# Optimization experiments

Hardware: AMD Instinct MI355X
Metric: run time of the kernel (lower is better)

The kernel has to match this reference:

```python
import jax, jax.numpy as jnp
import numpy as np

B, S, E = 4, 1024, 1024   # batch, seq_len, emb_dim
H = 8                      # num_head
D = E                      # in_emb_dim defaults to emb_dim
NEG = -9e15                # source uses -9000000000000000.0


def setup_inputs() -> dict:
    key = jax.random.key(0)
    kq, kk, kv, kwq, kwk, kwv, kwl = jax.random.split(key, 7)
    q = jax.random.normal(kq, (B, S, E), dtype=jnp.float32)
    k = jax.random.normal(kk, (B, S, E), dtype=jnp.float32)
    v = jax.random.normal(kv, (B, S, E), dtype=jnp.float32)
    # Per-head Linear(emb_dim -> in_emb_dim, bias=False) weights, torch layout [out, in]
    Wq = jax.random.normal(kwq, (H, D, E), dtype=jnp.float32) * 0.02
    Wk = jax.random.normal(kwk, (H, D, E), dtype=jnp.float32) * 0.02
    Wv = jax.random.normal(kwv, (H, D, E), dtype=jnp.float32) * 0.02
    # last_dense: Linear(in_emb_dim*num_head -> emb_dim, bias=False)
    Wlast = jax.random.normal(kwl, (E, H * D), dtype=jnp.float32) * 0.02
    return {"q": q, "k": k, "v": v, "Wq": Wq, "Wk": Wk, "Wv": Wv, "Wlast": Wlast}


def reference(q, k, v, Wq, Wk, Wv, Wlast):
    # batched per-head projections: y = x @ W[h].T  -> [B,H,S,D]
    in_q = jnp.einsum('bse,hde->bhsd', q, Wq)
    in_k = jnp.einsum('bse,hde->bhsd', k, Wk)
    in_v = jnp.einsum('bse,hde->bhsd', v, Wv)
    # faithful: scaled by sqrt(kv sequence length), not head dim
    scale = 1.0 / jnp.sqrt(jnp.float32(k.shape[-2]))
    logits = jnp.einsum('bhqd,bhkd->bhqk', in_q, in_k) * scale
    # source maps exactly-zero logits to -9e15 before softmax
    logits = jnp.where(logits != 0, logits, jnp.full_like(logits, NEG))
    atten = jax.nn.softmax(logits, axis=-1)          # [B,H,Sq,Sk]
    out_h = jnp.einsum('bhqk,bhkd->bhqd', atten, in_v)
    # concat heads along last dim in head order (matches torch.cat loop)
    b, h, sq, d = out_h.shape
    h_cat = out_h.transpose(0, 2, 1, 3).reshape(b, sq, h * d)
    return jnp.einsum('bsf,ef->bse', h_cat, Wlast)   # last_dense, bias=False
```

## Files before the change

### kernel.cpp

```cpp
#include <hip/hip_runtime.h>
#include <stdint.h>

typedef _Float16 f16;
typedef _Float16 f16x8 __attribute__((ext_vector_type(8)));
typedef _Float16 f16x4 __attribute__((ext_vector_type(4)));
typedef float f32x4 __attribute__((ext_vector_type(4)));

__device__ __forceinline__ void gload_lds16(const void* g, void* l) {
    __builtin_amdgcn_global_load_lds(
        (const __attribute__((address_space(1))) unsigned int*)g,
        (__attribute__((address_space(3))) unsigned int*)l, 16, 0, 0);
}

#define VMWAIT0() asm volatile("s_waitcnt vmcnt(0)" ::: "memory")
#define LGKM0()   asm volatile("s_waitcnt lgkmcnt(0)" ::: "memory")

struct Cvt3 {
    const float* s[3];
    f16* d[3];
};
__global__ __launch_bounds__(256) void cvt_plain3(Cvt3 c) {
    const int seg = blockIdx.y;
    const int i = blockIdx.x * 256 + threadIdx.x;
    const float4* s4 = (const float4*)c.s[seg];
    float4 a = s4[2 * (size_t)i];
    float4 b = s4[2 * (size_t)i + 1];
    f16x8 o;
    o[0] = (f16)a.x; o[1] = (f16)a.y; o[2] = (f16)a.z; o[3] = (f16)a.w;
    o[4] = (f16)b.x; o[5] = (f16)b.y; o[6] = (f16)b.z; o[7] = (f16)b.w;
    *(f16x8*)(c.d[seg] + (size_t)i * 8) = o;
}

__global__ __launch_bounds__(256) void cvt_wl(const float* __restrict__ s,
                                              f16* __restrict__ d) {
    const int i = blockIdx.x * 256 + threadIdx.x;
    const int d8 = i & 127;
    const int e  = (i >> 7) & 1023;
    const int h  = i >> 17;
    const float4* s4 = (const float4*)(s + (size_t)e * 8192 + h * 1024 + d8 * 8);
    float4 a = s4[0], b = s4[1];
    f16x8 o;
    o[0] = (f16)a.x; o[1] = (f16)a.y; o[2] = (f16)a.z; o[3] = (f16)a.w;
    o[4] = (f16)b.x; o[5] = (f16)b.y; o[6] = (f16)b.z; o[7] = (f16)b.w;
    *(f16x8*)(d + (size_t)i * 8) = o;
}

struct T3 { const float* s[3]; f16* d[3]; };
__global__ __launch_bounds__(256) void cvt_transpose3(T3 c) {
    const int bid = blockIdx.x;
    const int dt = bid & 15;
    const int et = (bid >> 4) & 15;
    const int zz = bid >> 8;
    const int m = zz >> 3, h = zz & 7;
    const float* src = c.s[m] + (size_t)h * 1048576;
    f16* dst = c.d[m] + (size_t)h * 1048576;
    __shared__ f16 t[64][72];
    const int r  = threadIdx.x >> 2;
    const int cq = threadIdx.x & 3;
    const int d0 = dt * 64, e0 = et * 64;
#pragma unroll
    for (int i = 0; i < 4; ++i) {
        const int cc = cq * 4 + i * 16;
        float4 vv = *(const float4*)(src + (size_t)(d0 + r) * 1024 + e0 + cc);
        t[cc + 0][r] = (f16)vv.x;
        t[cc + 1][r] = (f16)vv.y;
        t[cc + 2][r] = (f16)vv.z;
        t[cc + 3][r] = (f16)vv.w;
    }
    __syncthreads();
#pragma unroll
    for (int i = 0; i < 4; ++i) {
        const int cc = cq * 4 + i * 16;
        f16x4 w;
        w[0] = t[r][cc + 0];
        w[1] = t[r][cc + 1];
        w[2] = t[r][cc + 2];
        w[3] = t[r][cc + 3];
        *(f16x4*)(dst + (size_t)(e0 + r) * 1024 + d0 + cc) = w;
    }
}

template <typename OutT>
__global__ __launch_bounds__(256, 2) void gemm_bt(
    const f16* __restrict__ A, const f16* __restrict__ B, OutT* __restrict__ C,
    int ldA, int ldB, long long ldC, int K, float alpha,
    long long sAh, long long sAb, long long sBh, long long sBb,
    long long sCh, long long sCb, int NB, int gx, int gy) {
    const int nwg = gridDim.x;
    const int q = nwg >> 3, r = nwg & 7;
    const int xcd = blockIdx.x & 7, lid = blockIdx.x >> 3;
    const int wg = (xcd < r ? xcd * (q + 1) : r * (q + 1) + (xcd - r) * q) + lid;
    const int z = wg / (gx * gy);
    const int rem = wg - z * (gx * gy);
    const int by = rem / gx, bx = rem - by * gx;
    const int h = z / NB, bb = z % NB;
    A += h * sAh + bb * sAb;
    B += h * sBh + bb * sBb;
    C += h * sCh + bb * sCb;

    const int row0 = by * 128;
    const int col0 = bx * 128;

    __shared__ __align__(16) f16 smA[128 * 64];
    __shared__ __align__(16) f16 smB[128 * 64];

    const int tid  = threadIdx.x;
    const int lane = tid & 63;
    const int wid  = tid >> 6;
    const int wr   = (wid >> 1) * 64;
    const int wc   = (wid & 1) * 64;
    const int fr   = lane & 15;
    const int fkb  = (lane >> 4) * 16;

    f32x4 acc[4][4] = {};

    const int nkt = K >> 6;
    for (int kt = 0; kt < nkt; ++kt) {
#pragma unroll
        for (int it = 0; it < 4; ++it) {
            int p = (it * 256 + tid) * 16;
            int n = p ^ (((p >> 7) & 7) << 4);
            int rr  = n >> 7;
            int kel = (n & 127) >> 1;
            size_t ga = (size_t)(row0 + rr) * (size_t)ldA + (size_t)(kt * 64 + kel);
            gload_lds16(A + ga, (char*)smA + p);
            size_t gb = (size_t)(col0 + rr) * (size_t)ldB + (size_t)(kt * 64 + kel);
            gload_lds16(B + gb, (char*)smB + p);
        }
        __syncthreads();

#pragma unroll
        for (int ks = 0; ks < 2; ++ks) {
            f16x8 af[4], bf[4];
#pragma unroll
            for (int i = 0; i < 4; ++i) {
                int rowA = wr + i * 16 + fr;
                int na   = rowA * 128 + ks * 64 + fkb;
                af[i] = *(const f16x8*)((const char*)smA + (na ^ ((rowA & 7) << 4)));
                int rowB = wc + i * 16 + fr;
                int nb   = rowB * 128 + ks * 64 + fkb;
                bf[i] = *(const f16x8*)((const char*)smB + (nb ^ ((rowB & 7) << 4)));
            }
#pragma unroll
            for (int i = 0; i < 4; ++i)
#pragma unroll
                for (int j = 0; j < 4; ++j)
                    acc[i][j] = __builtin_amdgcn_mfma_f32_16x16x32_f16(
                        af[i], bf[j], acc[i][j], 0, 0, 0);
        }
        __syncthreads();
    }

    const int er = (lane >> 4) * 4;
#pragma unroll
    for (int i = 0; i < 4; ++i)
#pragma unroll
        for (int j = 0; j < 4; ++j)
#pragma unroll
            for (int rr = 0; rr < 4; ++rr) {
                size_t idx = (size_t)(row0 + wr + i * 16 + er + rr) * (size_t)ldC +
                             (size_t)(col0 + wc + j * 16 + fr);
                C[idx] = (OutT)(acc[i][j][rr] * alpha);
            }
}

template <typename OutT>
__global__ __launch_bounds__(512, 2) void gemm2ph(
    const f16* __restrict__ A, const f16* __restrict__ B, OutT* __restrict__ C,
    int ldA, int ldB, long long ldC, int K, float alpha,
    long long sAh, long long sAb, long long sBh, long long sBb,
    long long sCh, long long sCb, int NB, int gx, int gy) {
    extern __shared__ char lds[];

    const int nwg = gridDim.x;
    const int q = nwg >> 3, r = nwg & 7;
    const int xcd = blockIdx.x & 7, lid = blockIdx.x >> 3;
    const int wg = (xcd < r ? xcd * (q + 1) : r * (q + 1) + (xcd - r) * q) + lid;
    const int z = wg / (gx * gy);
    const int rem = wg - z * (gx * gy);
    const int by = rem / gx, bx = rem - by * gx;
    const int h = z / NB, bb = z - h * NB;
    A += h * sAh + bb * sAb;
    B += h * sBh + bb * sBb;
    C += h * sCh + bb * sCb;
    const int row0 = by * 256, col0 = bx * 256;

    const int tid  = threadIdx.x;
    const int lane = tid & 63;
    const int wid  = tid >> 6;
    const int wm   = wid >> 2;
    const int wn   = wid & 3;
    const int fr   = lane & 15;
    const int fkb  = (lane >> 4) << 4;
    const int sw0  = fkb ^ ((fr & 7) << 4);
    const int sw1  = sw0 ^ 64;

    const unsigned ldsbase = (unsigned)(uintptr_t)(char*)lds;
    const unsigned aRow = ldsbase + (unsigned)((wm * 128 + fr) * 128);
    const unsigned bRow = ldsbase + 32768u + (unsigned)((wn * 64 + fr) * 128);

    const int srow  = tid >> 3;
    const int scol  = (((tid & 7) ^ ((tid >> 3) & 7)) << 4) >> 1;
    const f16* gA = A + (size_t)(row0 + srow) * ldA + scol;
    const f16* gB = B + (size_t)(col0 + srow) * ldB + scol;
    char* lA = (char*)lds + tid * 16;
    char* lB = lA + 32768;

    const int nkt = K >> 6;

#define STAGE(tt, bufo) do { \
        const size_t _ko = (size_t)(tt) * 64; \
        gload_lds16(gA + _ko,                        lA + (bufo)); \
        gload_lds16(gA + 64  * (size_t)ldA + _ko,    lA + (bufo) + 8192); \
        gload_lds16(gA + 128 * (size_t)ldA + _ko,    lA + (bufo) + 16384); \
        gload_lds16(gA + 192 * (size_t)ldA + _ko,    lA + (bufo) + 24576); \
        gload_lds16(gB + _ko,                        lB + (bufo)); \
        gload_lds16(gB + 64  * (size_t)ldB + _ko,    lB + (bufo) + 8192); \
        gload_lds16(gB + 128 * (size_t)ldB + _ko,    lB + (bufo) + 16384); \
        gload_lds16(gB + 192 * (size_t)ldB + _ko,    lB + (bufo) + 24576); \
    } while (0)

#define DSR2(r0, r1, addr, o0, o1) \
    asm volatile("ds_read_b128 %0, %2 offset:" #o0 "\n\t" \
                 "ds_read_b128 %1, %2 offset:" #o1 \
                 : "=&v"(r0), "=&v"(r1) : "v"(addr))

#define MF(i, j, av, bv) \
    acc[i][j] = __builtin_amdgcn_mfma_f32_16x16x32_f16(av, bv, acc[i][j], 0, 0, 0)

#define HALF(sw) do { \
        f16x8 a0, a1, a2, a3, a4, a5, a6, a7, b0, b1, b2, b3; \
        const unsigned aA = aRow + bo + (sw); \
        const unsigned aB = bRow + bo + (sw); \
        DSR2(a0, a1, aA, 0, 2048); \
        DSR2(a2, a3, aA, 4096, 6144); \
        DSR2(a4, a5, aA, 8192, 10240); \
        DSR2(a6, a7, aA, 12288, 14336); \
        DSR2(b0, b1, aB, 0, 2048); \
        DSR2(b2, b3, aB, 4096, 6144); \
        LGKM0(); \
        __builtin_amdgcn_sched_barrier(0); \
        __builtin_amdgcn_s_setprio(1); \
        MF(0,0,a0,b0); MF(0,1,a0,b1); MF(0,2,a0,b2); MF(0,3,a0,b3); \
        MF(1,0,a1,b0); MF(1,1,a1,b1); MF(1,2,a1,b2); MF(1,3,a1,b3); \
        MF(2,0,a2,b0); MF(2,1,a2,b1); MF(2,2,a2,b2); MF(2,3,a2,b3); \
        MF(3,0,a3,b0); MF(3,1,a3,b1); MF(3,2,a3,b2); MF(3,3,a3,b3); \
        MF(4,0,a4,b0); MF(4,1,a4,b1); MF(4,2,a4,b2); MF(4,3,a4,b3); \
        MF(5,0,a5,b0); MF(5,1,a5,b1); MF(5,2,a5,b2); MF(5,3,a5,b3); \
        MF(6,0,a6,b0); MF(6,1,a6,b1); MF(6,2,a6,b2); MF(6,3,a6,b3); \
        MF(7,0,a7,b0); MF(7,1,a7,b1); MF(7,2,a7,b2); MF(7,3,a7,b3); \
        __builtin_amdgcn_s_setprio(0); \
    } while (0)

    STAGE(0, 0);
    VMWAIT0();
    __builtin_amdgcn_s_barrier();

    f32x4 acc[8][4] = {};
    unsigned cur = 0;

    for (int t = 0; t < nkt; ++t) {
        const unsigned bo = cur << 16;
        if (t + 1 < nkt) STAGE(t + 1, bo ^ 65536u);
        HALF(sw0);
        HALF(sw1);
        VMWAIT0();
        __builtin_amdgcn_s_barrier();
        cur ^= 1;
    }
#undef HALF
#undef MF
#undef DSR2
#undef STAGE

    const int er = (lane >> 4) * 4;
#pragma unroll
    for (int i = 0; i < 8; ++i)
#pragma unroll
        for (int j = 0; j < 4; ++j)
#pragma unroll
            for (int rr = 0; rr < 4; ++rr) {
                size_t idx = (size_t)(row0 + wm * 128 + i * 16 + er + rr) * (size_t)ldC +
                             (size_t)(col0 + wn * 64 + j * 16 + fr);
                C[idx] = (OutT)(acc[i][j][rr] * alpha);
            }
}

__global__ __launch_bounds__(256) void reduce_split2(const float* __restrict__ p,
                                                     float* __restrict__ o, int n4) {
    int i = blockIdx.x * 256 + threadIdx.x;
    if (i >= n4) return;
    const int b  = i >> 18;
    const int jj = i & 262143;
    const float4* p4 = (const float4*)p;
    const size_t base = (size_t)b * 524288 + jj;
    float4 a = p4[base], c = p4[base + 262144];
    float4 s;
    s.x = a.x + c.x;
    s.y = a.y + c.y;
    s.z = a.z + c.z;
    s.w = a.w + c.w;
    ((float4*)o)[i] = s;
}

__global__ __launch_bounds__(256) void softmax_rows(f16* __restrict__ P) {
    const size_t row = blockIdx.x;
    f16* p = P + row * 1024;
    const int tid = threadIdx.x, lane = tid & 63, wid = tid >> 6;

    f16x4 v4 = *(const f16x4*)(p + tid * 4);
    float v[4];
#pragma unroll
    for (int t = 0; t < 4; ++t) {
        v[t] = (float)v4[t];
        if (v[t] == 0.0f) v[t] = -9e15f;
    }
    float m = fmaxf(fmaxf(v[0], v[1]), fmaxf(v[2], v[3]));
#pragma unroll
    for (int o = 32; o > 0; o >>= 1) m = fmaxf(m, __shfl_xor(m, o));
    __shared__ float red[8];
    if (lane == 0) red[wid] = m;
    __syncthreads();
    m = fmaxf(fmaxf(red[0], red[1]), fmaxf(red[2], red[3]));

    float e[4], s = 0.f;
#pragma unroll
    for (int t = 0; t < 4; ++t) { e[t] = __expf(v[t] - m); s += e[t]; }
#pragma unroll
    for (int o = 32; o > 0; o >>= 1) s += __shfl_xor(s, o);
    if (lane == 0) red[4 + wid] = s;
    __syncthreads();
    s = red[4] + red[5] + red[6] + red[7];
    float inv = 1.0f / s;

    f16x4 o4;
#pragma unroll
    for (int t = 0; t < 4; ++t) o4[t] = (f16)(e[t] * inv);
    *(f16x4*)(p + tid * 4) = o4;
}

extern "C" void kernel_launch(void* const* d_in, const int* in_sizes, int n_in,
                              void* d_out, int out_size, void* d_ws, size_t ws_size,
                              hipStream_t stream) {
    const float* q  = (const float*)d_in[0];
    const float* k  = (const float*)d_in[1];
    const float* v  = (const float*)d_in[2];
    const float* Wq = (const float*)d_in[3];
    const float* Wk = (const float*)d_in[4];
    const float* Wv = (const float*)d_in[5];
    const float* Wl = (const float*)d_in[6];
    float* out = (float*)d_out;

    (void)hipFuncSetAttribute((const void*)gemm2ph<f16>,
                              hipFuncAttributeMaxDynamicSharedMemorySize, 131072);

    const size_t MB = 1024ull * 1024ull;
    char* ws = (char*)d_ws;
    f16*  q_h  = (f16*)(ws + 0 * MB);
    f16*  k_h  = (f16*)(ws + 8 * MB);
    f16*  v_h  = (f16*)(ws + 16 * MB);
    f16*  WkT  = (f16*)(ws + 24 * MB);
    f16*  Wl_r = (f16*)(ws + 40 * MB);
    f16*  WqT  = (f16*)(ws + 56 * MB);
    f16*  WvT  = (f16*)(ws + 72 * MB);
    f16*  Mt   = (f16*)(ws + 88 * MB);
    f16*  G    = (f16*)(ws + 104 * MB);
    f16*  Aq   = (f16*)(ws + 24 * MB);
    f16*  P    = (f16*)(ws + 120 * MB);
    f16*  Xt   = (f16*)(ws + 24 * MB);
    float* part = (float*)(ws + 88 * MB);

    Cvt3 c3;
    c3.s[0] = q;  c3.d[0] = q_h;
    c3.s[1] = k;  c3.d[1] = k_h;
    c3.s[2] = v;  c3.d[2] = v_h;
    cvt_plain3<<<dim3(2048, 3), 256, 0, stream>>>(c3);
    cvt_wl<<<4096, 256, 0, stream>>>(Wl, Wl_r);

    T3 t3;
    t3.s[0] = Wq; t3.d[0] = WqT;
    t3.s[1] = Wk; t3.d[1] = WkT;
    t3.s[2] = Wv; t3.d[2] = WvT;
    cvt_transpose3<<<6144, 256, 0, stream>>>(t3);

    const long long M1 = 1048576ll;
    const long long M8 = 8388608ll;
    const float SCALE = 0.03125f;
    const size_t SMEM = 131072;

    gemm2ph<f16><<<256, 512, SMEM, stream>>>(
        WkT, WqT, Mt, 1024, 1024, 1024, 1024, 1.0f,
        M1, 0, M1, 0, M1, 0, 1, 4, 4);
    gemm2ph<f16><<<512, 512, SMEM, stream>>>(
        q_h, Mt, Aq, 1024, 1024, 1024, 1024, 1.0f,
        0, M1, M1, 0, 4 * M1, M1, 4, 4, 4);
    gemm2ph<f16><<<512, 512, SMEM, stream>>>(
        Aq, k_h, P, 1024, 1024, 8192, 1024, SCALE,
        4 * M1, M1, 0, M1, 1024, M8, 4, 4, 4);
    gemm2ph<f16><<<512, 512, SMEM, stream>>>(
        G, v_h, Xt, 1024, 1024, 8192, 1024, 1.0f,
        M1, 0, 0, M1, 1024, M8, 4, 4, 4);
    softmax_rows<<<32768, 256, 0, stream>>>(P);
    gemm_bt<float><<<512, 256, 0, stream>>>(
        P, Xt, part, 8192, 8192, 1024, 4096, 1.0f,
        M8, 4096, M8, 4096, 2 * M1, M1, 2, 8, 8);
    reduce_split2<<<4096, 256, 0, stream>>>(part, out, 1048576);
}
```

Measured before the change: 397.5 us.

## Merge conversion kernels, use one-wave-per-row softmax, switch Wk·Wq GEMM kernel

```diff
diff --git a/kernel.cpp b/kernel.cpp
--- a/kernel.cpp
+++ b/kernel.cpp
@@ -15,34 +15,30 @@
 #define VMWAIT0() asm volatile("s_waitcnt vmcnt(0)" ::: "memory")
 #define LGKM0()   asm volatile("s_waitcnt lgkmcnt(0)" ::: "memory")
 
-struct Cvt3 {
-    const float* s[3];
-    f16* d[3];
+struct CvtAll {
+    const float* s[4];
+    f16* d[4];
 };
-__global__ __launch_bounds__(256) void cvt_plain3(Cvt3 c) {
+__global__ __launch_bounds__(256) void cvt_all(CvtAll c) {
     const int seg = blockIdx.y;
     const int i = blockIdx.x * 256 + threadIdx.x;
-    const float4* s4 = (const float4*)c.s[seg];
-    float4 a = s4[2 * (size_t)i];
-    float4 b = s4[2 * (size_t)i + 1];
-    f16x8 o;
-    o[0] = (f16)a.x; o[1] = (f16)a.y; o[2] = (f16)a.z; o[3] = (f16)a.w;
-    o[4] = (f16)b.x; o[5] = (f16)b.y; o[6] = (f16)b.z; o[7] = (f16)b.w;
-    *(f16x8*)(c.d[seg] + (size_t)i * 8) = o;
-}
-
-__global__ __launch_bounds__(256) void cvt_wl(const float* __restrict__ s,
-                                              f16* __restrict__ d) {
-    const int i = blockIdx.x * 256 + threadIdx.x;
-    const int d8 = i & 127;
-    const int e  = (i >> 7) & 1023;
-    const int h  = i >> 17;
-    const float4* s4 = (const float4*)(s + (size_t)e * 8192 + h * 1024 + d8 * 8);
+    const float* sp;
+    f16* dp = c.d[seg] + (size_t)i * 8;
+    if (seg < 3) {
+        if (i >= 524288) return;
+        sp = c.s[seg] + (size_t)i * 8;
+    } else {
+        const int d8 = i & 127;
+        const int e  = (i >> 7) & 1023;
+        const int h  = i >> 17;
+        sp = c.s[3] + (size_t)e * 8192 + h * 1024 + d8 * 8;
+    }
+    const float4* s4 = (const float4*)sp;
     float4 a = s4[0], b = s4[1];
     f16x8 o;
     o[0] = (f16)a.x; o[1] = (f16)a.y; o[2] = (f16)a.z; o[3] = (f16)a.w;
     o[4] = (f16)b.x; o[5] = (f16)b.y; o[6] = (f16)b.z; o[7] = (f16)b.w;
-    *(f16x8*)(d + (size_t)i * 8) = o;
+    *(f16x8*)dp = o;
 }
 
 struct T3 { const float* s[3]; f16* d[3]; };
@@ -304,39 +300,42 @@
 }
 
 __global__ __launch_bounds__(256) void softmax_rows(f16* __restrict__ P) {
-    const size_t row = blockIdx.x;
-    f16* p = P + row * 1024;
-    const int tid = threadIdx.x, lane = tid & 63, wid = tid >> 6;
-
-    f16x4 v4 = *(const f16x4*)(p + tid * 4);
-    float v[4];
-#pragma unroll
-    for (int t = 0; t < 4; ++t) {
-        v[t] = (float)v4[t];
+    const int wid = threadIdx.x >> 6, lane = threadIdx.x & 63;
+    const size_t row = (size_t)blockIdx.x * 4 + wid;
+    f16* p = P + row * 1024 + lane * 16;
+
+    f16x8 u0 = *(const f16x8*)p;
+    f16x8 u1 = *(const f16x8*)(p + 8);
+    float v[16];
+#pragma unroll
+    for (int t = 0; t < 8; ++t) {
+        v[t]     = (float)u0[t];
+        v[t + 8] = (float)u1[t];
+    }
+#pragma unroll
+    for (int t = 0; t < 16; ++t)
         if (v[t] == 0.0f) v[t] = -9e15f;
-    }
-    float m = fmaxf(fmaxf(v[0], v[1]), fmaxf(v[2], v[3]));
+
+    float m = v[0];
+#pragma unroll
+    for (int t = 1; t < 16; ++t) m = fmaxf(m, v[t]);
 #pragma unroll
     for (int o = 32; o > 0; o >>= 1) m = fmaxf(m, __shfl_xor(m, o));
-    __shared__ float red[8];
-    if (lane == 0) red[wid] = m;
-    __syncthreads();
-    m = fmaxf(fmaxf(red[0], red[1]), fmaxf(red[2], red[3]));
-
-    float e[4], s = 0.f;
-#pragma unroll
-    for (int t = 0; t < 4; ++t) { e[t] = __expf(v[t] - m); s += e[t]; }
+
+    float e[16], s = 0.f;
+#pragma unroll
+    for (int t = 0; t < 16; ++t) { e[t] = __expf(v[t] - m); s += e[t]; }
 #pragma unroll
     for (int o = 32; o > 0; o >>= 1) s += __shfl_xor(s, o);
-    if (lane == 0) red[4 + wid] = s;
-    __syncthreads();
-    s = red[4] + red[5] + red[6] + red[7];
-    float inv = 1.0f / s;
-
-    f16x4 o4;
-#pragma unroll
-    for (int t = 0; t < 4; ++t) o4[t] = (f16)(e[t] * inv);
-    *(f16x4*)(p + tid * 4) = o4;
+    const float inv = 1.0f / s;
+
+#pragma unroll
+    for (int t = 0; t < 8; ++t) {
+        u0[t] = (f16)(e[t] * inv);
+        u1[t] = (f16)(e[t + 8] * inv);
+    }
+    *(f16x8*)p = u0;
+    *(f16x8*)(p + 8) = u1;
 }
 
 extern "C" void kernel_launch(void* const* d_in, const int* in_sizes, int n_in,
@@ -370,12 +369,12 @@
     f16*  Xt   = (f16*)(ws + 24 * MB);
     float* part = (float*)(ws + 88 * MB);
 
-    Cvt3 c3;
-    c3.s[0] = q;  c3.d[0] = q_h;
-    c3.s[1] = k;  c3.d[1] = k_h;
-    c3.s[2] = v;  c3.d[2] = v_h;
-    cvt_plain3<<<dim3(2048, 3), 256, 0, stream>>>(c3);
-    cvt_wl<<<4096, 256, 0, stream>>>(Wl, Wl_r);
+    CvtAll ca;
+    ca.s[0] = q;  ca.d[0] = q_h;
+    ca.s[1] = k;  ca.d[1] = k_h;
+    ca.s[2] = v;  ca.d[2] = v_h;
+    ca.s[3] = Wl; ca.d[3] = Wl_r;
+    cvt_all<<<dim3(4096, 4), 256, 0, stream>>>(ca);
 
     T3 t3;
     t3.s[0] = Wq; t3.d[0] = WqT;
@@ -388,9 +387,9 @@
     const float SCALE = 0.03125f;
     const size_t SMEM = 131072;
 
-    gemm2ph<f16><<<256, 512, SMEM, stream>>>(
+    gemm_bt<f16><<<1024, 256, 0, stream>>>(
         WkT, WqT, Mt, 1024, 1024, 1024, 1024, 1.0f,
-        M1, 0, M1, 0, M1, 0, 1, 4, 4);
+        M1, 0, M1, 0, M1, 0, 1, 8, 8);
     gemm2ph<f16><<<512, 512, SMEM, stream>>>(
         q_h, Mt, Aq, 1024, 1024, 1024, 1024, 1.0f,
         0, M1, M1, 0, 4 * M1, M1, 4, 4, 4);
@@ -400,7 +399,7 @@
     gemm2ph<f16><<<512, 512, SMEM, stream>>>(
         G, v_h, Xt, 1024, 1024, 8192, 1024, 1.0f,
         M1, 0, 0, M1, 1024, M8, 4, 4, 4);
-    softmax_rows<<<32768, 256, 0, stream>>>(P);
+    softmax_rows<<<8192, 256, 0, stream>>>(P);
     gemm_bt<float><<<512, 256, 0, stream>>>(
         P, Xt, part, 8192, 8192, 1024, 4096, 1.0f,
         M8, 4096, M8, 4096, 2 * M1, M1, 2, 8, 8);
```

Result: slower. 408.2 us, median of 2 (+2.7%).
